# Performance work log

Hardware: AMD Instinct MI355X
Metric: run time of the kernel (lower is better)

The kernel has to match this reference:

```python
import jax, jax.numpy as jnp
import numpy as np

N = 100_000   # nodes
E = 1_600_000 # directed edges
G = 2048      # graphs in batch
NF = 78       # input node features
DIM = 32      # GIN hidden dim
L = 5         # num GIN layers
OUT = 128     # output_dim
BN_EPS = 1e-5


def setup_inputs() -> dict:
    key = jax.random.key(0)
    ks = jax.random.split(key, 8)
    s = 0.1
    return {
        "x": jax.random.normal(ks[0], (N, NF), jnp.float32),
        "edge_index": jax.random.randint(ks[1], (2, E), 0, N, jnp.int32),
        "batch": jnp.sort(jax.random.randint(ks[2], (N,), 0, G, jnp.int32)),
        "W1_0": (jax.random.normal(ks[3], (NF, DIM), jnp.float32) * s),
        "W1_rest": (jax.random.normal(ks[4], (L - 1, DIM, DIM), jnp.float32) * s),
        "b1": jnp.zeros((L, DIM), jnp.float32),
        "W2": (jax.random.normal(ks[5], (L, DIM, DIM), jnp.float32) * s),
        "b2": jnp.zeros((L, DIM), jnp.float32),
        "gamma": jnp.ones((L, DIM), jnp.float32),
        "beta": jnp.zeros((L, DIM), jnp.float32),
        "Wfc": (jax.random.normal(ks[6], (DIM, OUT), jnp.float32) * s),
        "bfc": jnp.zeros((OUT,), jnp.float32),
    }


def reference(x, edge_index, batch, W1_0, W1_rest, b1, W2, b2, gamma, beta, Wfc, bfc):
    src, dst = edge_index[0], edge_index[1]
    h = x
    for i in range(L):
        # GINConv (eps=0): h_i' = MLP(h_i + sum_{j->i} h_j)
        agg = jax.ops.segment_sum(h[src], dst, num_segments=N)  # [N, d]
        h = h + agg
        W1 = W1_0 if i == 0 else W1_rest[i - 1]
        h = jnp.maximum(h @ W1 + b1[i], 0.0) @ W2[i] + b2[i]
        # ReLU then BatchNorm1d (training mode: batch stats, biased var)
        h = jnp.maximum(h, 0.0)
        mu = h.mean(axis=0)
        var = h.var(axis=0)
        h = gamma[i] * (h - mu) * jax.lax.rsqrt(var + BN_EPS) + beta[i]
    pooled = jax.ops.segment_sum(h, batch, num_segments=G)  # global_add_pool [G, DIM]
    return jnp.maximum(pooled @ Wfc + bfc, 0.0)  # dropout is identity (eval)
```

## Files before the change

kernel.cpp:

```cpp
#include <hip/hip_runtime.h>
#include <hip/hip_fp16.h>

#define N_NODES 100000
#define N_EDGES 1600000
#define N_GRAPHS 2048
#define NFEAT 78
#define DIM 32
#define NLAYERS 5
#define OUTD 128
#define BN_EPS 1e-5f
#define NPB 32
#define NBUK 391
#define BNODES 256
#define STRIDE 4608
#define EPB 2048
#define NBLK ((N_EDGES + EPB - 1) / EPB)
#define NSLOT 16
#define PSTRIDE (NSLOT * 2 * DIM)

__device__ __forceinline__ float2 up2(unsigned u) {
    __half2 h = *reinterpret_cast<__half2*>(&u);
    return __half22float2(h);
}
__device__ __forceinline__ unsigned pk2(float a, float b) {
    __half2 h = __floats2half2_rn(a, b);
    return *reinterpret_cast<unsigned*>(&h);
}

__global__ __launch_bounds__(256) void prep_kernel(
    const int* __restrict__ ei, int* __restrict__ bcnt, int* __restrict__ bdata,
    const float* __restrict__ x, const float* __restrict__ W1_0,
    unsigned short* __restrict__ y)
{
    __shared__ int cur[NBUK];
    __shared__ int gbl[NBUK];
    __shared__ float Wl[NFEAT * DIM];
    int tid = threadIdx.x;

    if (blockIdx.x < NBLK) {
        int base = blockIdx.x * EPB;
        for (int i = tid; i < NBUK; i += 256) cur[i] = 0;
        __syncthreads();

        int ew[8], eb[8];
        const int4* s4 = (const int4*)ei;
        const int4* d4 = (const int4*)(ei + N_EDGES);
#pragma unroll
        for (int c = 0; c < 2; ++c) {
            int eidx = base + c * 1024 + tid * 4;
            if (eidx < N_EDGES) {
                int4 sv = s4[eidx >> 2];
                int4 dv = d4[eidx >> 2];
                ew[c*4+0] = sv.x | ((dv.x & 255) << 17); eb[c*4+0] = dv.x >> 8;
                ew[c*4+1] = sv.y | ((dv.y & 255) << 17); eb[c*4+1] = dv.y >> 8;
                ew[c*4+2] = sv.z | ((dv.z & 255) << 17); eb[c*4+2] = dv.z >> 8;
                ew[c*4+3] = sv.w | ((dv.w & 255) << 17); eb[c*4+3] = dv.w >> 8;
            } else {
                eb[c*4+0] = eb[c*4+1] = eb[c*4+2] = eb[c*4+3] = -1;
                ew[c*4+0] = ew[c*4+1] = ew[c*4+2] = ew[c*4+3] = 0;
            }
        }
        int slot[8];
#pragma unroll
        for (int k = 0; k < 8; ++k)
            slot[k] = (eb[k] >= 0) ? atomicAdd(&cur[eb[k]], 1) : 0;
        __syncthreads();
        for (int b = tid; b < NBUK; b += 256) {
            int c = cur[b];
            gbl[b] = (c > 0) ? atomicAdd(&bcnt[b], c) : 0;
        }
        __syncthreads();
#pragma unroll
        for (int k = 0; k < 8; ++k) {
            int b = eb[k];
            if (b >= 0) {
                int pos = gbl[b] + slot[k];
                if (pos < STRIDE) bdata[b * STRIDE + pos] = ew[k];
            }
        }
    } else {
        for (int i = tid; i < NFEAT * DIM; i += 256) Wl[i] = W1_0[i];
        __syncthreads();
        int t = (blockIdx.x - NBLK) * 256 + tid;
        int row = t >> 3;
        int c0 = (t & 7) * 4;
        float a0 = 0.f, a1 = 0.f, a2 = 0.f, a3 = 0.f;
        const float* hr = x + (long)row * NFEAT;
        for (int k = 0; k < NFEAT; ++k) {
            float xv = hr[k];
            a0 = fmaf(xv, Wl[k * DIM + c0 + 0], a0);
            a1 = fmaf(xv, Wl[k * DIM + c0 + 1], a1);
            a2 = fmaf(xv, Wl[k * DIM + c0 + 2], a2);
            a3 = fmaf(xv, Wl[k * DIM + c0 + 3], a3);
        }
        ((uint2*)y)[(long)row * 8 + (t & 7)] = make_uint2(pk2(a0, a1), pk2(a2, a3));
    }
}

__global__ __launch_bounds__(512) void bscan_kernel(
    const int* __restrict__ bcnt, int* __restrict__ bbase)
{
    __shared__ int sd[512];
    int t = threadIdx.x;
    int v = (t < NBUK) ? min(bcnt[t], STRIDE) : 0;
    sd[t] = v; __syncthreads();
    for (int off = 1; off < 512; off <<= 1) {
        int a = (t >= off) ? sd[t - off] : 0;
        __syncthreads();
        sd[t] += a;
        __syncthreads();
    }
    if (t < NBUK) bbase[t + 1] = sd[t];
    if (t == 0) bbase[0] = 0;
}

__global__ __launch_bounds__(256) void cfill2_kernel(
    const int* __restrict__ bcnt, const int* __restrict__ bbase,
    const int* __restrict__ bdata, int* __restrict__ edge_src,
    int* __restrict__ offs, int* __restrict__ ghist)
{
    __shared__ int sorted[STRIDE];
    __shared__ int cnt[BNODES], off[BNODES], cur[BNODES];
    __shared__ int lhist[64];
    int b = blockIdx.x, tid = threadIdx.x;
    int n = min(bcnt[b], STRIDE);
    int gb = bbase[b];
    const int* slab = bdata + (long)b * STRIDE;

    if (tid < BNODES) cnt[tid] = 0;
    if (tid < 64) lhist[tid] = 0;
    __syncthreads();
    for (int i = tid; i < n; i += 256)
        atomicAdd(&cnt[slab[i] >> 17], 1);
    __syncthreads();
    int t = tid;
    if (t < BNODES) off[t] = cnt[t];
    __syncthreads();
    for (int o = 1; o < BNODES; o <<= 1) {
        int a = (t >= o && t < BNODES) ? off[t - o] : 0;
        __syncthreads();
        if (t < BNODES) off[t] += a;
        __syncthreads();
    }
    if (t < BNODES) {
        int excl = off[t] - cnt[t];
        off[t] = excl;
        cur[t] = excl;
        int node = b * BNODES + t;
        if (node <= N_NODES) offs[node] = gb + excl;
        if (node < N_NODES) atomicAdd(&lhist[min(cnt[t], 63)], 1);
    }
    __syncthreads();
    if (tid < 64) {
        int h = lhist[tid];
        if (h) atomicAdd(&ghist[tid], h);
    }
    for (int i = tid; i < n; i += 256) {
        int w = slab[i];
        int pos = atomicAdd(&cur[w >> 17], 1);
        sorted[pos] = w & 0x1FFFF;
    }
    __syncthreads();
    for (int i = tid; i < n; i += 256)
        edge_src[gb + i] = sorted[i];
}

__global__ __launch_bounds__(64) void dscan_kernel(
    const int* __restrict__ ghist, int* __restrict__ binCursor)
{
    __shared__ int sd[64];
    int t = threadIdx.x;
    int v = ghist[t];
    sd[t] = v; __syncthreads();
    for (int off = 1; off < 64; off <<= 1) {
        int a = (t >= off) ? sd[t - off] : 0;
        __syncthreads();
        sd[t] += a;
        __syncthreads();
    }
    binCursor[t] = sd[t] - v;
}

__global__ __launch_bounds__(256) void dfill_kernel(
    const int* __restrict__ offs, int* __restrict__ binCursor,
    int* __restrict__ perm)
{
    __shared__ int lhist[64], lbase[64], lcur[64];
    int tid = threadIdx.x;
    int node = blockIdx.x * 256 + tid;
    if (tid < 64) { lhist[tid] = 0; lcur[tid] = 0; }
    __syncthreads();
    int bin = -1;
    if (node < N_NODES) {
        int d = offs[node + 1] - offs[node];
        bin = min(d, 63);
        atomicAdd(&lhist[bin], 1);
    }
    __syncthreads();
    if (tid < 64) {
        int c = lhist[tid];
        lbase[tid] = c ? atomicAdd(&binCursor[tid], c) : 0;
    }
    __syncthreads();
    if (bin >= 0) {
        int p = atomicAdd(&lcur[bin], 1);
        perm[lbase[bin] + p] = node;
    }
}

template<bool MM>
__global__ __launch_bounds__(256) void layer_kernel(
    const int* __restrict__ perm,
    const int* __restrict__ offs, const int* __restrict__ edge_src,
    const unsigned short* __restrict__ zin,
    const float* __restrict__ W1g,
    const float* __restrict__ partial_prev,
    const float* __restrict__ gprev, const float* __restrict__ bprev,
    const float* __restrict__ b1v,
    const float* __restrict__ W2, const float* __restrict__ b2v,
    unsigned short* __restrict__ zout, float* __restrict__ partial)
{
    __shared__ float W1l[DIM * DIM];
    __shared__ float W2l[DIM * DIM];
    __shared__ float zs[NPB][36];
    __shared__ float b1l[DIM], b2l[DIM], cl[DIM];
    __shared__ float sscl[DIM], sshl[DIM];
    __shared__ float psum[DIM], psq[DIM];

    int tid = threadIdx.x;
    float* red = &zs[0][0];

    for (int i = tid; i < DIM * DIM; i += 256) W2l[i] = W2[i];
    if (tid < DIM) {
        b1l[tid] = b1v[tid]; b2l[tid] = b2v[tid];
        psum[tid] = 0.f; psq[tid] = 0.f;
    }
    if (MM) {
        int c = tid & 63, chunk = tid >> 6;
        float a = 0.f;
        for (int p = chunk; p < NSLOT; p += 4) a += partial_prev[p * 64 + c];
        red[tid] = a;
        __syncthreads();
        if (tid < 64) red[tid] = red[tid] + red[tid+64] + red[tid+128] + red[tid+192];
        __syncthreads();
        if (tid < DIM) {
            const float invN = 1.0f / (float)N_NODES;
            float S = red[tid], Q = red[tid + DIM];
            float mu = S * invN;
            float var = Q * invN - mu * mu;
            float sc = gprev[tid] * rsqrtf(var + BN_EPS);
            sscl[tid] = sc;
            sshl[tid] = bprev[tid] - mu * sc;
        }
        __syncthreads();
        for (int i = tid; i < DIM * DIM; i += 256) W1l[i] = sscl[i >> 5] * W1g[i];
        if (tid < DIM) {
            float cv = 0.f;
            for (int k = 0; k < DIM; ++k) cv = fmaf(sshl[k], W1g[k * DIM + tid], cv);
            cl[tid] = cv;
        }
    }
    __syncthreads();

    int ln = tid >> 3, p = tid & 7;
    int c0 = p * 4;
    int node = perm[blockIdx.x * NPB + ln];
    int beg = offs[node], end = offs[node + 1];
    int deg = end - beg;
    const uint2* zb = (const uint2*)zin;

    uint2 sv = zb[(long)node * 8 + p];
    float2 f;
    f = up2(sv.x); float a0 = f.x, a1 = f.y;
    f = up2(sv.y); float a2 = f.x, a3 = f.y;
    int e = beg;
    for (; e + 8 <= end; e += 8) {
        uint2 v0 = zb[(long)edge_src[e + 0] * 8 + p];
        uint2 v1 = zb[(long)edge_src[e + 1] * 8 + p];
        uint2 v2 = zb[(long)edge_src[e + 2] * 8 + p];
        uint2 v3 = zb[(long)edge_src[e + 3] * 8 + p];
        uint2 v4 = zb[(long)edge_src[e + 4] * 8 + p];
        uint2 v5 = zb[(long)edge_src[e + 5] * 8 + p];
        uint2 v6 = zb[(long)edge_src[e + 6] * 8 + p];
        uint2 v7 = zb[(long)edge_src[e + 7] * 8 + p];
        f = up2(v0.x); a0 += f.x; a1 += f.y;  f = up2(v0.y); a2 += f.x; a3 += f.y;
        f = up2(v1.x); a0 += f.x; a1 += f.y;  f = up2(v1.y); a2 += f.x; a3 += f.y;
        f = up2(v2.x); a0 += f.x; a1 += f.y;  f = up2(v2.y); a2 += f.x; a3 += f.y;
        f = up2(v3.x); a0 += f.x; a1 += f.y;  f = up2(v3.y); a2 += f.x; a3 += f.y;
        f = up2(v4.x); a0 += f.x; a1 += f.y;  f = up2(v4.y); a2 += f.x; a3 += f.y;
        f = up2(v5.x); a0 += f.x; a1 += f.y;  f = up2(v5.y); a2 += f.x; a3 += f.y;
        f = up2(v6.x); a0 += f.x; a1 += f.y;  f = up2(v6.y); a2 += f.x; a3 += f.y;
        f = up2(v7.x); a0 += f.x; a1 += f.y;  f = up2(v7.y); a2 += f.x; a3 += f.y;
    }
    for (; e < end; ++e) {
        uint2 v = zb[(long)edge_src[e] * 8 + p];
        f = up2(v.x); a0 += f.x; a1 += f.y;
        f = up2(v.y); a2 += f.x; a3 += f.y;
    }
    *(float4*)&zs[ln][c0] = make_float4(a0, a1, a2, a3);

    float t4[4];
    if (MM) {
        t4[0] = t4[1] = t4[2] = t4[3] = 0.f;
#pragma unroll
        for (int k = 0; k < DIM; ++k) {
            float zk = zs[ln][k];
            t4[0] = fmaf(zk, W1l[k * DIM + c0 + 0], t4[0]);
            t4[1] = fmaf(zk, W1l[k * DIM + c0 + 1], t4[1]);
            t4[2] = fmaf(zk, W1l[k * DIM + c0 + 2], t4[2]);
            t4[3] = fmaf(zk, W1l[k * DIM + c0 + 3], t4[3]);
        }
        float dp1 = (float)(deg + 1);
#pragma unroll
        for (int j = 0; j < 4; ++j)
            t4[j] = fmaxf(fmaf(dp1, cl[c0 + j], t4[j]) + b1l[c0 + j], 0.f);
    } else {
        t4[0] = fmaxf(a0 + b1l[c0 + 0], 0.f);
        t4[1] = fmaxf(a1 + b1l[c0 + 1], 0.f);
        t4[2] = fmaxf(a2 + b1l[c0 + 2], 0.f);
        t4[3] = fmaxf(a3 + b1l[c0 + 3], 0.f);
    }
    *(float4*)&zs[ln][c0] = make_float4(t4[0], t4[1], t4[2], t4[3]);

    float zv[4] = { b2l[c0 + 0], b2l[c0 + 1], b2l[c0 + 2], b2l[c0 + 3] };
#pragma unroll
    for (int k = 0; k < DIM; ++k) {
        float sk = zs[ln][k];
        zv[0] = fmaf(sk, W2l[k * DIM + c0 + 0], zv[0]);
        zv[1] = fmaf(sk, W2l[k * DIM + c0 + 1], zv[1]);
        zv[2] = fmaf(sk, W2l[k * DIM + c0 + 2], zv[2]);
        zv[3] = fmaf(sk, W2l[k * DIM + c0 + 3], zv[3]);
    }
#pragma unroll
    for (int j = 0; j < 4; ++j) zv[j] = fmaxf(zv[j], 0.f);
    ((uint2*)zout)[(long)node * 8 + p] = make_uint2(pk2(zv[0], zv[1]), pk2(zv[2], zv[3]));

    float sq[4];
#pragma unroll
    for (int j = 0; j < 4; ++j) sq[j] = zv[j] * zv[j];
#pragma unroll
    for (int off = 8; off < 64; off <<= 1) {
#pragma unroll
        for (int j = 0; j < 4; ++j) {
            zv[j] += __shfl_xor(zv[j], off, 64);
            sq[j] += __shfl_xor(sq[j], off, 64);
        }
    }
    if ((tid & 63) < 8) {
#pragma unroll
        for (int j = 0; j < 4; ++j) {
            atomicAdd(&psum[c0 + j], zv[j]);
            atomicAdd(&psq[c0 + j], sq[j]);
        }
    }
    __syncthreads();
    if (tid < 2 * DIM) {
        float v = (tid < DIM) ? psum[tid] : psq[tid - DIM];
        atomicAdd(&partial[(blockIdx.x & (NSLOT - 1)) * 2 * DIM + tid], v);
    }
}

__global__ __launch_bounds__(256) void pool_kernel(
    const unsigned short* __restrict__ z, const int* __restrict__ batch,
    float* __restrict__ praw, float* __restrict__ cntg)
{
    __shared__ float acc[32][32];
    __shared__ float cntL[32];
    __shared__ int slot[32];
    __shared__ int segg[32];
    __shared__ int nsegS;
    int tid = threadIdx.x;
    for (int i = tid; i < 1024; i += 256) ((float*)acc)[i] = 0.f;
    if (tid < 32) cntL[tid] = 0.f;
    int nodeBase = blockIdx.x * 32;
    if (tid < 32) {
        int nd = nodeBase + tid;
        int gv = batch[nd];
        int flag = (tid == 0) ? 1 : (gv != batch[nd - 1]);
        unsigned long long m = __ballot(flag);
        int s = __popcll(m & ((2ull << tid) - 1ull)) - 1;
        slot[tid] = s;
        if (flag) segg[s] = gv;
        if (tid == 0) nsegS = __popcll(m);
    }
    __syncthreads();

    int ln = tid >> 3;
    int p = tid & 7;
    long node = nodeBase + ln;
    uint2 u = ((const uint2*)z)[node * 8 + p];
    int c = p * 4;
    float2 f01 = up2(u.x), f23 = up2(u.y);
    int s = slot[ln];
    atomicAdd(&acc[s][c+0], f01.x);
    atomicAdd(&acc[s][c+1], f01.y);
    atomicAdd(&acc[s][c+2], f23.x);
    atomicAdd(&acc[s][c+3], f23.y);
    if (p == 0) atomicAdd(&cntL[s], 1.f);
    __syncthreads();

    int total = nsegS * 32;
    for (int i = tid; i < total; i += 256) {
        int r = i >> 5, dd = i & 31;
        float val = acc[r][dd];
        if (val != 0.f) atomicAdd(&praw[(long)segg[r] * DIM + dd], val);
    }
    if (tid < nsegS) atomicAdd(&cntg[segg[tid]], cntL[tid]);
}

__global__ __launch_bounds__(256) void fc_kernel(
    const float* __restrict__ praw, const float* __restrict__ cntg,
    const float* __restrict__ partial4,
    const float* __restrict__ g4, const float* __restrict__ be4,
    const float* __restrict__ Wfc, const float* __restrict__ bfc,
    float* __restrict__ out)
{
    __shared__ float Wl[DIM * OUTD];
    __shared__ float red[256];
    __shared__ float sscl[DIM], sshl[DIM], dvec[OUTD];
    int tid = threadIdx.x;
    for (int i = tid; i < DIM * OUTD; i += 256) Wl[i] = Wfc[i];
    {
        int c = tid & 63, chunk = tid >> 6;
        float a = 0.f;
        for (int p = chunk; p < NSLOT; p += 4) a += partial4[p * 64 + c];
        red[tid] = a;
    }
    __syncthreads();
    if (tid < 64) red[tid] = red[tid] + red[tid+64] + red[tid+128] + red[tid+192];
    __syncthreads();
    if (tid < DIM) {
        const float invN = 1.0f / (float)N_NODES;
        float S = red[tid], Q = red[tid + DIM];
        float mu = S * invN;
        float var = Q * invN - mu * mu;
        float sc = g4[tid] * rsqrtf(var + BN_EPS);
        sscl[tid] = sc;
        sshl[tid] = be4[tid] - mu * sc;
    }
    __syncthreads();
    if (tid < OUTD) {
        float dv = 0.f;
        for (int k = 0; k < DIM; ++k) dv = fmaf(sshl[k], Wl[k * OUTD + tid], dv);
        dvec[tid] = dv;
    }
    __syncthreads();
    int t = blockIdx.x * 256 + tid;
    int g = t >> 7;
    int o = t & (OUTD - 1);
    float acc = bfc[o] + cntg[g] * dvec[o];
    const float* pr = praw + (long)g * DIM;
#pragma unroll
    for (int k = 0; k < DIM; ++k)
        acc = fmaf(sscl[k] * pr[k], Wl[k * OUTD + o], acc);
    out[t] = fmaxf(acc, 0.f);
}

extern "C" void kernel_launch(void* const* d_in, const int* in_sizes, int n_in,
                              void* d_out, int out_size, void* d_ws, size_t ws_size,
                              hipStream_t stream) {
    const float* x      = (const float*)d_in[0];
    const int*   ei     = (const int*)  d_in[1];
    const int*   batch  = (const int*)  d_in[2];
    const float* W1_0   = (const float*)d_in[3];
    const float* W1_rest= (const float*)d_in[4];
    const float* b1     = (const float*)d_in[5];
    const float* W2     = (const float*)d_in[6];
    const float* b2     = (const float*)d_in[7];
    const float* gamma  = (const float*)d_in[8];
    const float* beta   = (const float*)d_in[9];
    const float* Wfc    = (const float*)d_in[10];
    const float* bfc    = (const float*)d_in[11];
    float* out = (float*)d_out;

    int* wsi = (int*)d_ws;
    const size_t nf = (size_t)N_NODES * DIM;
    const size_t BD = (size_t)NBUK * STRIDE;
    int*   bdata  = wsi;
    unsigned short* zfpA = (unsigned short*)(wsi + BD);
    unsigned short* zfpB = zfpA + nf;
    int*   edge_src = (int*)(zfpB + nf);
    int*   offs   = edge_src + N_EDGES;
    int*   perm   = offs + (N_NODES + 1);
    int*   bcnt   = perm + N_NODES;
    int*   ghist  = bcnt + NBUK;
    int*   binCursor = ghist + 64;
    int*   bbase  = binCursor + 64;
    float* praw   = (float*)(bbase + NBUK + 1);
    float* cntg   = praw + (size_t)N_GRAPHS * DIM;
    float* partial= cntg + N_GRAPHS;

    hipMemsetAsync(praw, 0,
        ((size_t)N_GRAPHS * DIM + N_GRAPHS + NLAYERS * PSTRIDE) * sizeof(float),
        stream);
    hipMemsetAsync(bcnt, 0, (size_t)(NBUK + 64) * sizeof(int), stream);

    const int grpBlocks = (N_NODES * 8) / 256;

    prep_kernel<<<NBLK + grpBlocks, 256, 0, stream>>>(
        ei, bcnt, bdata, x, W1_0, zfpA);
    bscan_kernel<<<1, 512, 0, stream>>>(bcnt, bbase);
    cfill2_kernel<<<NBUK, 256, 0, stream>>>(
        bcnt, bbase, bdata, edge_src, offs, ghist);
    dscan_kernel<<<1, 64, 0, stream>>>(ghist, binCursor);
    dfill_kernel<<<(N_NODES + 255) / 256, 256, 0, stream>>>(offs, binCursor, perm);

    layer_kernel<false><<<N_NODES / NPB, 256, 0, stream>>>(
        perm, offs, edge_src, zfpA, nullptr, nullptr, nullptr, nullptr,
        b1, W2, b2, zfpB, partial);

    const unsigned short* zi = zfpB;
    unsigned short* zo = zfpA;
    for (int i = 1; i < NLAYERS; ++i) {
        layer_kernel<true><<<N_NODES / NPB, 256, 0, stream>>>(
            perm, offs, edge_src, zi,
            W1_rest + (size_t)(i - 1) * DIM * DIM,
            partial + (size_t)(i - 1) * PSTRIDE,
            gamma + (i - 1) * DIM, beta + (i - 1) * DIM,
            b1 + i * DIM, W2 + (size_t)i * DIM * DIM, b2 + i * DIM,
            zo, partial + (size_t)i * PSTRIDE);
        const unsigned short* tmp = zi; zi = zo; zo = (unsigned short*)tmp;
    }

    pool_kernel<<<N_NODES / 32, 256, 0, stream>>>(zi, batch, praw, cntg);
    fc_kernel<<<(N_GRAPHS * OUTD) / 256, 256, 0, stream>>>(
        praw, cntg, partial + (size_t)(NLAYERS - 1) * PSTRIDE,
        gamma + (NLAYERS - 1) * DIM, beta + (NLAYERS - 1) * DIM,
        Wfc, bfc, out);
}
```

Baseline: 315.2 us.

## Drop bucket scan kernel via atomic cursor and per-bucket offsets; double edges per block

Removes the single-block bucket prefix-scan launch. Each bucket block now claims its global edge range with an atomic cursor, and node offsets are stored in a padded per-bucket layout (257 entries per bucket) that dfill and the layer kernels index by bucket. Separately, the prep kernel now handles 4096 edges per block instead of 2048, halving the edge-block count at the cost of more registers per thread. Edge ranges are no longer in bucket order, but each node's range stays contiguous.

```diff
diff --git a/kernel.cpp b/kernel.cpp
--- a/kernel.cpp
+++ b/kernel.cpp
@@ -13,10 +13,11 @@
 #define NBUK 391
 #define BNODES 256
 #define STRIDE 4608
-#define EPB 2048
+#define EPB 4096
 #define NBLK ((N_EDGES + EPB - 1) / EPB)
 #define NSLOT 16
 #define PSTRIDE (NSLOT * 2 * DIM)
+#define OSTR (BNODES + 1)
 
 __device__ __forceinline__ float2 up2(unsigned u) {
     __half2 h = *reinterpret_cast<__half2*>(&u);
@@ -42,11 +43,11 @@
         for (int i = tid; i < NBUK; i += 256) cur[i] = 0;
         __syncthreads();
 
-        int ew[8], eb[8];
+        int ew[16], eb[16];
         const int4* s4 = (const int4*)ei;
         const int4* d4 = (const int4*)(ei + N_EDGES);
 #pragma unroll
-        for (int c = 0; c < 2; ++c) {
+        for (int c = 0; c < 4; ++c) {
             int eidx = base + c * 1024 + tid * 4;
             if (eidx < N_EDGES) {
                 int4 sv = s4[eidx >> 2];
@@ -60,9 +61,9 @@
                 ew[c*4+0] = ew[c*4+1] = ew[c*4+2] = ew[c*4+3] = 0;
             }
         }
-        int slot[8];
-#pragma unroll
-        for (int k = 0; k < 8; ++k)
+        int slot[16];
+#pragma unroll
+        for (int k = 0; k < 16; ++k)
             slot[k] = (eb[k] >= 0) ? atomicAdd(&cur[eb[k]], 1) : 0;
         __syncthreads();
         for (int b = tid; b < NBUK; b += 256) {
@@ -71,7 +72,7 @@
         }
         __syncthreads();
 #pragma unroll
-        for (int k = 0; k < 8; ++k) {
+        for (int k = 0; k < 16; ++k) {
             int b = eb[k];
             if (b >= 0) {
                 int pos = gbl[b] + slot[k];
@@ -97,39 +98,24 @@
     }
 }
 
-__global__ __launch_bounds__(512) void bscan_kernel(
-    const int* __restrict__ bcnt, int* __restrict__ bbase)
-{
-    __shared__ int sd[512];
-    int t = threadIdx.x;
-    int v = (t < NBUK) ? min(bcnt[t], STRIDE) : 0;
-    sd[t] = v; __syncthreads();
-    for (int off = 1; off < 512; off <<= 1) {
-        int a = (t >= off) ? sd[t - off] : 0;
-        __syncthreads();
-        sd[t] += a;
-        __syncthreads();
-    }
-    if (t < NBUK) bbase[t + 1] = sd[t];
-    if (t == 0) bbase[0] = 0;
-}
-
 __global__ __launch_bounds__(256) void cfill2_kernel(
-    const int* __restrict__ bcnt, const int* __restrict__ bbase,
-    const int* __restrict__ bdata, int* __restrict__ edge_src,
-    int* __restrict__ offs, int* __restrict__ ghist)
+    const int* __restrict__ bcnt, const int* __restrict__ bdata,
+    int* __restrict__ edge_src, int* __restrict__ offsB,
+    int* __restrict__ ghist, int* __restrict__ gcursor)
 {
     __shared__ int sorted[STRIDE];
     __shared__ int cnt[BNODES], off[BNODES], cur[BNODES];
     __shared__ int lhist[64];
+    __shared__ int gbS;
     int b = blockIdx.x, tid = threadIdx.x;
     int n = min(bcnt[b], STRIDE);
-    int gb = bbase[b];
     const int* slab = bdata + (long)b * STRIDE;
 
+    if (tid == 0) gbS = atomicAdd(gcursor, n);
     if (tid < BNODES) cnt[tid] = 0;
     if (tid < 64) lhist[tid] = 0;
     __syncthreads();
+    int gb = gbS;
     for (int i = tid; i < n; i += 256)
         atomicAdd(&cnt[slab[i] >> 17], 1);
     __syncthreads();
@@ -146,10 +132,11 @@
         int excl = off[t] - cnt[t];
         off[t] = excl;
         cur[t] = excl;
+        offsB[b * OSTR + t] = gb + excl;
         int node = b * BNODES + t;
-        if (node <= N_NODES) offs[node] = gb + excl;
         if (node < N_NODES) atomicAdd(&lhist[min(cnt[t], 63)], 1);
     }
+    if (tid == 0) offsB[b * OSTR + BNODES] = gb + n;
     __syncthreads();
     if (tid < 64) {
         int h = lhist[tid];
@@ -182,7 +169,7 @@
 }
 
 __global__ __launch_bounds__(256) void dfill_kernel(
-    const int* __restrict__ offs, int* __restrict__ binCursor,
+    const int* __restrict__ offsB, int* __restrict__ binCursor,
     int* __restrict__ perm)
 {
     __shared__ int lhist[64], lbase[64], lcur[64];
@@ -192,7 +179,8 @@
     __syncthreads();
     int bin = -1;
     if (node < N_NODES) {
-        int d = offs[node + 1] - offs[node];
+        int b = node >> 8, t = node & 255;
+        int d = offsB[b * OSTR + t + 1] - offsB[b * OSTR + t];
         bin = min(d, 63);
         atomicAdd(&lhist[bin], 1);
     }
@@ -211,7 +199,7 @@
 template<bool MM>
 __global__ __launch_bounds__(256) void layer_kernel(
     const int* __restrict__ perm,
-    const int* __restrict__ offs, const int* __restrict__ edge_src,
+    const int* __restrict__ offsB, const int* __restrict__ edge_src,
     const unsigned short* __restrict__ zin,
     const float* __restrict__ W1g,
     const float* __restrict__ partial_prev,
@@ -265,7 +253,8 @@
     int ln = tid >> 3, p = tid & 7;
     int c0 = p * 4;
     int node = perm[blockIdx.x * NPB + ln];
-    int beg = offs[node], end = offs[node + 1];
+    int ob = (node >> 8) * OSTR + (node & 255);
+    int beg = offsB[ob], end = offsB[ob + 1];
     int deg = end - beg;
     const uint2* zb = (const uint2*)zin;
 
@@ -480,40 +469,39 @@
     unsigned short* zfpA = (unsigned short*)(wsi + BD);
     unsigned short* zfpB = zfpA + nf;
     int*   edge_src = (int*)(zfpB + nf);
-    int*   offs   = edge_src + N_EDGES;
-    int*   perm   = offs + (N_NODES + 1);
+    int*   offsB  = edge_src + N_EDGES;
+    int*   perm   = offsB + NBUK * OSTR;
     int*   bcnt   = perm + N_NODES;
     int*   ghist  = bcnt + NBUK;
-    int*   binCursor = ghist + 64;
-    int*   bbase  = binCursor + 64;
-    float* praw   = (float*)(bbase + NBUK + 1);
+    int*   gcursor= ghist + 64;
+    int*   binCursor = gcursor + 1;
+    float* praw   = (float*)(binCursor + 64);
     float* cntg   = praw + (size_t)N_GRAPHS * DIM;
     float* partial= cntg + N_GRAPHS;
 
     hipMemsetAsync(praw, 0,
         ((size_t)N_GRAPHS * DIM + N_GRAPHS + NLAYERS * PSTRIDE) * sizeof(float),
         stream);
-    hipMemsetAsync(bcnt, 0, (size_t)(NBUK + 64) * sizeof(int), stream);
+    hipMemsetAsync(bcnt, 0, (size_t)(NBUK + 64 + 1) * sizeof(int), stream);
 
     const int grpBlocks = (N_NODES * 8) / 256;
 
     prep_kernel<<<NBLK + grpBlocks, 256, 0, stream>>>(
         ei, bcnt, bdata, x, W1_0, zfpA);
-    bscan_kernel<<<1, 512, 0, stream>>>(bcnt, bbase);
     cfill2_kernel<<<NBUK, 256, 0, stream>>>(
-        bcnt, bbase, bdata, edge_src, offs, ghist);
+        bcnt, bdata, edge_src, offsB, ghist, gcursor);
     dscan_kernel<<<1, 64, 0, stream>>>(ghist, binCursor);
-    dfill_kernel<<<(N_NODES + 255) / 256, 256, 0, stream>>>(offs, binCursor, perm);
+    dfill_kernel<<<(N_NODES + 255) / 256, 256, 0, stream>>>(offsB, binCursor, perm);
 
     layer_kernel<false><<<N_NODES / NPB, 256, 0, stream>>>(
-        perm, offs, edge_src, zfpA, nullptr, nullptr, nullptr, nullptr,
+        perm, offsB, edge_src, zfpA, nullptr, nullptr, nullptr, nullptr,
         b1, W2, b2, zfpB, partial);
 
     const unsigned short* zi = zfpB;
     unsigned short* zo = zfpA;
     for (int i = 1; i < NLAYERS; ++i) {
         layer_kernel<true><<<N_NODES / NPB, 256, 0, stream>>>(
-            perm, offs, edge_src, zi,
+            perm, offsB, edge_src, zi,
             W1_rest + (size_t)(i - 1) * DIM * DIM,
             partial + (size_t)(i - 1) * PSTRIDE,
             gamma + (i - 1) * DIM, beta + (i - 1) * DIM,
```

Result: faster. 301.1 us (-4.5%).
